# Performance work log

Hardware: AMD Instinct MI355X
Metric: run time of the kernel (lower is better)

Reference implementation:

```python
import jax, jax.numpy as jnp
import numpy as np

SR = 48000          # sample_rate
N = 24000           # num_samples (0.5 s)
NOISE_CUTOFF = 0.1  # torch.tensor([0.1]) in TransientGenerator


def exponential_envelope(n, attack, decay):
    # attack ramp times exponential decay over normalized time in [0, 1]
    t = jnp.linspace(0.0, 1.0, n)
    return (1.0 - jnp.exp(-attack * t)) * jnp.exp(-decay * t)


def one_pole_filter(x, cutoff):
    # y[n] = cutoff * x[n] + (1 - cutoff) * y[n-1]  (one-pole lowpass)
    def step(y, xi):
        y = cutoff * xi + (1.0 - cutoff) * y
        return y, y
    _, ys = jax.lax.scan(step, jnp.zeros((), x.dtype), x)
    return ys


def _drum_synth(parameters, noise_t, noise_n):
    t = jnp.linspace(0.0, 1.0, N)

    # ---- TransientGenerator (parameters[:5]) ----
    # params: attack (unused in original forward), decay, frequency, saturation, gain
    decay_t = parameters[1]
    freq_t = parameters[2]
    sat = parameters[3]
    gain_t = parameters[4]
    sine = jnp.sin(2.0 * jnp.pi * freq_t * t) * jnp.exp(-decay_t * t) * gain_t
    sine = jnp.tanh(sine * sat)
    filtered = one_pole_filter(noise_t, NOISE_CUTOFF)
    noise_comp = filtered * jnp.exp(-(decay_t * 20.0) * t) * (gain_t / 2.0)
    transient = sine + noise_comp  # [N]

    # ---- Resonator (parameters[5:8]): fractional-delay feedback recurrence ----
    freq_r = parameters[5]
    feedback = parameters[6]
    gain_r = parameters[7]
    delay_samples = SR / freq_r
    delayed = jnp.arange(N, dtype=jnp.float32) - delay_samples
    valid = (delayed >= 0).astype(jnp.float32)
    fl = jnp.clip(jnp.floor(delayed).astype(jnp.int32), 0, N - 1)
    ce = jnp.clip(fl + 1, 0, N - 1)
    frac = delayed - fl.astype(jnp.float32)  # computed after clamp, as in original

    out0 = jnp.zeros((N,), transient.dtype).at[0].set(transient[0])
    idx = jnp.arange(1, N, dtype=jnp.int32)

    def step(out, x):
        i, f_i, c_i, fr_i, vm_i, tr_i = x
        interp = (1.0 - fr_i) * out[f_i] + fr_i * out[c_i]
        out = out.at[i].set(tr_i + feedback * interp * vm_i)
        return out, None

    out, _ = jax.lax.scan(
        step, out0, (idx, fl[1:], ce[1:], frac[1:], valid[1:], transient[1:]))
    resonance = out * gain_r

    # ---- NoiseGenerator (parameters[8:]) ----
    attack_n = parameters[8]
    decay_n = parameters[9]
    gain_n = parameters[10]
    env = exponential_envelope(N, attack_n, decay_n)
    noise = noise_n * env * gain_n

    return transient + noise + resonance


def setup_inputs() -> dict:
    key = jax.random.key(0)
    k1, k2 = jax.random.split(key)
    # [attack_t, decay_t, freq_t, saturation, gain_t,
    #  freq_res, feedback, gain_res, attack_n, decay_n, gain_n]
    parameters = jnp.array(
        [0.01, 8.0, 60.0, 2.0, 1.0, 150.0, 0.95, 0.8, 50.0, 10.0, 0.3],
        dtype=jnp.float32)
    noise_t = jax.random.normal(k1, (N,), dtype=jnp.float32)
    noise_n = jax.random.normal(k2, (N,), dtype=jnp.float32)
    return {"parameters": parameters, "noise_t": noise_t, "noise_n": noise_n}


def reference(parameters, noise_t, noise_n):
    return _drum_synth(parameters, noise_t, noise_n)
```

## Files before the change

### kernel.cpp

```cpp
#include <hip/hip_runtime.h>
#include <math.h>


constexpr int   kN    = 24000;
constexpr float kInvT = 1.0f / 23999.0f;
constexpr int   kBT   = 64;

__global__ __launch_bounds__(kBT) void k1_transient(
    const float* __restrict__ params,
    const float* __restrict__ noise_t,
    float* __restrict__ tr)
{
  const int i = blockIdx.x * kBT + threadIdx.x;
  if (i >= kN) return;

  const float decay_t = params[1];
  const float freq_t  = params[2];
  const float sat     = params[3];
  const float gain_t  = params[4];

  float p0 = 0.f, p1 = 0.f, p2 = 0.f, p3 = 0.f;
  if (i >= 63) {
    #pragma unroll
    for (int j = 15; j >= 0; --j) {
      const int b = i - j;
      p0 = fmaf(0.9f, p0, noise_t[b     ]);
      p1 = fmaf(0.9f, p1, noise_t[b - 16]);
      p2 = fmaf(0.9f, p2, noise_t[b - 32]);
      p3 = fmaf(0.9f, p3, noise_t[b - 48]);
    }
  } else {
    #pragma unroll
    for (int j = 15; j >= 0; --j) {
      const int b = i - j;
      p0 = fmaf(0.9f, p0, (b      >= 0) ? noise_t[b     ] : 0.0f);
      p1 = fmaf(0.9f, p1, (b - 16 >= 0) ? noise_t[b - 16] : 0.0f);
      p2 = fmaf(0.9f, p2, (b - 32 >= 0) ? noise_t[b - 32] : 0.0f);
      p3 = fmaf(0.9f, p3, (b - 48 >= 0) ? noise_t[b - 48] : 0.0f);
    }
  }
  const float filtered = 0.1f * (p0 + 0.185302019f * p1
                                    + 0.034336838f * p2
                                    + 0.006362685f * p3);

  const float t = (float)i * kInvT;
  float s = __sinf(6.28318530718f * freq_t * t) * __expf(-decay_t * t) * gain_t;
  const float e2 = __expf(2.0f * sat * s);
  s = 1.0f - 2.0f / (e2 + 1.0f);
  const float nc = filtered * __expf(-decay_t * 20.0f * t) * (gain_t * 0.5f);
  tr[i] = s + nc;
}

__global__ __launch_bounds__(kBT) void k2_combine(
    const float* __restrict__ params,
    const float* __restrict__ noise_n,
    const float* __restrict__ tr,
    float* __restrict__ res_ws,
    float* __restrict__ out)
{
  const float fb  = params[6];
  const float gr  = params[7];
  const float att = params[8];
  const float dec = params[9];
  const float gn  = params[10];

  const float Dd = 48000.0f / params[5];
  const float fD = floorf(Dd);
  const int   B  = (int)fD;

  if (Dd == fD && B >= 1) {
    const int i = blockIdx.x * kBT + threadIdx.x;
    if (i >= kN) return;

    const float fb3 = fb * fb * fb;
    float res;

    if (B >= 320) {
      float p0 = 0.f, p1 = 0.f, p2 = 0.f;
      #pragma unroll
      for (int j = 24; j >= 0; --j) {
        const int i0 = i - 3 * j * B;
        const int i1 = i0 - B;
        const int i2 = i1 - B;
        p0 = fmaf(fb3, p0, (i0 >= 0) ? tr[i0] : 0.0f);
        p1 = fmaf(fb3, p1, (i1 >= 0) ? tr[i1] : 0.0f);
        p2 = fmaf(fb3, p2, (i2 >= 0) ? tr[i2] : 0.0f);
      }
      res = p0 + fb * p1 + (fb * fb) * p2;
    } else {
      const int Mmax = (kN - 1) / B;
      const int J    = Mmax / 3 + 1;
      float p0 = 0.f, p1 = 0.f, p2 = 0.f;
      for (int j = J - 1; j >= 0; --j) {
        const int i0 = i - 3 * j * B;
        const int i1 = i0 - B;
        const int i2 = i1 - B;
        p0 = fmaf(fb3, p0, (i0 >= 0) ? tr[i0] : 0.0f);
        p1 = fmaf(fb3, p1, (i1 >= 0) ? tr[i1] : 0.0f);
        p2 = fmaf(fb3, p2, (i2 >= 0) ? tr[i2] : 0.0f);
      }
      res = p0 + fb * p1 + (fb * fb) * p2;
    }

    const float t   = (float)i * kInvT;
    const float env = (1.0f - __expf(-att * t)) * __expf(-dec * t);
    out[i] = tr[i] + noise_n[i] * env * gn + gr * res;
  } else {
    if (blockIdx.x != 0) return;
    const int tid = threadIdx.x;
    const int Bb = (B < 1) ? 1 : B;
    const int nBands = (kN + Bb - 1) / Bb;
    for (int k = 0; k < nBands; ++k) {
      const int start = k * Bb;
      const int end = (start + Bb < kN) ? (start + Bb) : kN;
      if (tid == 0) {
        const int i = start;
        const float delayed = (float)i - Dd;
        const float validf = (delayed >= 0.0f) ? 1.0f : 0.0f;
        int fl = (int)floorf(delayed);
        fl = fl < 0 ? 0 : (fl > kN - 1 ? kN - 1 : fl);
        const int ce = fl + 1 > kN - 1 ? kN - 1 : fl + 1;
        const float frac = delayed - (float)fl;
        const float vfl = (fl <= start - 1) ? res_ws[fl] : 0.0f;
        const float vce = (ce <= start - 1) ? res_ws[ce] : 0.0f;
        res_ws[i] = tr[i] + fb * ((1.0f - frac) * vfl + frac * vce) * validf;
      }
      __syncthreads();
      for (int i = start + 1 + tid; i < end; i += kBT) {
        const float delayed = (float)i - Dd;
        const float validf = (delayed >= 0.0f) ? 1.0f : 0.0f;
        int fl = (int)floorf(delayed);
        fl = fl < 0 ? 0 : (fl > kN - 1 ? kN - 1 : fl);
        const int ce = fl + 1 > kN - 1 ? kN - 1 : fl + 1;
        const float frac = delayed - (float)fl;
        const float vfl = (fl <= start) ? res_ws[fl] : 0.0f;
        const float vce = (ce <= start) ? res_ws[ce] : 0.0f;
        res_ws[i] = tr[i] + fb * ((1.0f - frac) * vfl + frac * vce) * validf;
      }
      __syncthreads();
    }
    for (int i = tid; i < kN; i += kBT) {
      const float t   = (float)i * kInvT;
      const float env = (1.0f - __expf(-att * t)) * __expf(-dec * t);
      out[i] = tr[i] + noise_n[i] * env * gn + gr * res_ws[i];
    }
  }
}

extern "C" void kernel_launch(void* const* d_in, const int* in_sizes, int n_in,
                              void* d_out, int out_size, void* d_ws, size_t ws_size,
                              hipStream_t stream) {
  const float* params  = (const float*)d_in[0];
  const float* noise_t = (const float*)d_in[1];
  const float* noise_n = (const float*)d_in[2];
  float* out = (float*)d_out;
  float* ws_tr  = (float*)d_ws;
  float* ws_res = (float*)d_ws + kN;

  const int nb = (kN + kBT - 1) / kBT;
  k1_transient<<<nb, kBT, 0, stream>>>(params, noise_t, ws_tr);
  k2_combine<<<nb, kBT, 0, stream>>>(params, noise_n, ws_tr, ws_res, out);
}
```

Before: 63.01 us.

## Fuse transient and resonator kernels by recomputing transient at delayed taps

Merges the two kernels into one. Each thread recomputes the sine and filtered-noise transient terms at every delayed tap of its comb sum instead of reading a precomputed transient buffer. The noise term is truncated past a cutoff index where its exponential envelope is negligible, so the costly FIR evaluation runs only over a limited range of taps. This removes a kernel launch and the intermediate global buffer round trip, at the cost of much more redundant transcendental and FIR work per output and a small approximation from the truncation.

```diff
diff --git a/kernel.cpp b/kernel.cpp
--- a/kernel.cpp
+++ b/kernel.cpp
@@ -6,112 +6,120 @@
 constexpr float kInvT = 1.0f / 23999.0f;
 constexpr int   kBT   = 64;
 
-__global__ __launch_bounds__(kBT) void k1_transient(
+__device__ __forceinline__ float fir_filtered(const float* __restrict__ x, int k) {
+  float p0 = 0.f, p1 = 0.f, p2 = 0.f, p3 = 0.f;
+  if (k >= 63) {
+    #pragma unroll
+    for (int j = 15; j >= 0; --j) {
+      const int b = k - j;
+      p0 = fmaf(0.9f, p0, x[b     ]);
+      p1 = fmaf(0.9f, p1, x[b - 16]);
+      p2 = fmaf(0.9f, p2, x[b - 32]);
+      p3 = fmaf(0.9f, p3, x[b - 48]);
+    }
+  } else {
+    #pragma unroll
+    for (int j = 15; j >= 0; --j) {
+      const int b = k - j;
+      p0 = fmaf(0.9f, p0, (b      >= 0) ? x[b     ] : 0.0f);
+      p1 = fmaf(0.9f, p1, (b - 16 >= 0) ? x[b - 16] : 0.0f);
+      p2 = fmaf(0.9f, p2, (b - 32 >= 0) ? x[b - 32] : 0.0f);
+      p3 = fmaf(0.9f, p3, (b - 48 >= 0) ? x[b - 48] : 0.0f);
+    }
+  }
+  return 0.1f * (p0 + 0.185302019f * p1 + 0.034336838f * p2 + 0.006362685f * p3);
+}
+
+__device__ __forceinline__ float sine_part(int k, float decay_t, float freq_t,
+                                           float sat, float gain_t) {
+  const float t = (float)k * kInvT;
+  float s = __sinf(6.28318530718f * freq_t * t) * __expf(-decay_t * t) * gain_t;
+  const float e2 = __expf(2.0f * sat * s);
+  return 1.0f - 2.0f / (e2 + 1.0f);
+}
+
+__device__ __forceinline__ float noise_part(const float* __restrict__ noise_t,
+                                            int k, float decay_t, float gain_t) {
+  return fir_filtered(noise_t, k)
+       * __expf(-decay_t * 20.0f * (float)k * kInvT) * (gain_t * 0.5f);
+}
+
+__global__ __launch_bounds__(kBT) void k_fused(
     const float* __restrict__ params,
     const float* __restrict__ noise_t,
-    float* __restrict__ tr)
+    const float* __restrict__ noise_n,
+    float* __restrict__ ws_tr,
+    float* __restrict__ res_ws,
+    float* __restrict__ out)
 {
-  const int i = blockIdx.x * kBT + threadIdx.x;
-  if (i >= kN) return;
-
   const float decay_t = params[1];
   const float freq_t  = params[2];
   const float sat     = params[3];
   const float gain_t  = params[4];
-
-  float p0 = 0.f, p1 = 0.f, p2 = 0.f, p3 = 0.f;
-  if (i >= 63) {
-    #pragma unroll
-    for (int j = 15; j >= 0; --j) {
-      const int b = i - j;
-      p0 = fmaf(0.9f, p0, noise_t[b     ]);
-      p1 = fmaf(0.9f, p1, noise_t[b - 16]);
-      p2 = fmaf(0.9f, p2, noise_t[b - 32]);
-      p3 = fmaf(0.9f, p3, noise_t[b - 48]);
-    }
-  } else {
-    #pragma unroll
-    for (int j = 15; j >= 0; --j) {
-      const int b = i - j;
-      p0 = fmaf(0.9f, p0, (b      >= 0) ? noise_t[b     ] : 0.0f);
-      p1 = fmaf(0.9f, p1, (b - 16 >= 0) ? noise_t[b - 16] : 0.0f);
-      p2 = fmaf(0.9f, p2, (b - 32 >= 0) ? noise_t[b - 32] : 0.0f);
-      p3 = fmaf(0.9f, p3, (b - 48 >= 0) ? noise_t[b - 48] : 0.0f);
-    }
-  }
-  const float filtered = 0.1f * (p0 + 0.185302019f * p1
-                                    + 0.034336838f * p2
-                                    + 0.006362685f * p3);
-
-  const float t = (float)i * kInvT;
-  float s = __sinf(6.28318530718f * freq_t * t) * __expf(-decay_t * t) * gain_t;
-  const float e2 = __expf(2.0f * sat * s);
-  s = 1.0f - 2.0f / (e2 + 1.0f);
-  const float nc = filtered * __expf(-decay_t * 20.0f * t) * (gain_t * 0.5f);
-  tr[i] = s + nc;
-}
-
-__global__ __launch_bounds__(kBT) void k2_combine(
-    const float* __restrict__ params,
-    const float* __restrict__ noise_n,
-    const float* __restrict__ tr,
-    float* __restrict__ res_ws,
-    float* __restrict__ out)
-{
-  const float fb  = params[6];
-  const float gr  = params[7];
-  const float att = params[8];
-  const float dec = params[9];
-  const float gn  = params[10];
+  const float fb      = params[6];
+  const float gr      = params[7];
+  const float att     = params[8];
+  const float dec     = params[9];
+  const float gn      = params[10];
 
   const float Dd = 48000.0f / params[5];
   const float fD = floorf(Dd);
   const int   B  = (int)fD;
 
+  int kcut = kN;
+  if (decay_t > 0.0f) {
+    const float kc = 16.118f / (20.0f * decay_t) * 23999.0f;
+    kcut = (kc >= (float)kN) ? kN : ((int)kc + 1);
+  }
+
   if (Dd == fD && B >= 1) {
     const int i = blockIdx.x * kBT + threadIdx.x;
     if (i >= kN) return;
 
-    const float fb3 = fb * fb * fb;
-    float res;
+    const int Mmax = i / B;
+    int mlo = 0;
+    if (i - kcut + 1 > 0) mlo = (i - kcut + B) / B;
 
-    if (B >= 320) {
-      float p0 = 0.f, p1 = 0.f, p2 = 0.f;
-      #pragma unroll
-      for (int j = 24; j >= 0; --j) {
-        const int i0 = i - 3 * j * B;
-        const int i1 = i0 - B;
-        const int i2 = i1 - B;
-        p0 = fmaf(fb3, p0, (i0 >= 0) ? tr[i0] : 0.0f);
-        p1 = fmaf(fb3, p1, (i1 >= 0) ? tr[i1] : 0.0f);
-        p2 = fmaf(fb3, p2, (i2 >= 0) ? tr[i2] : 0.0f);
-      }
-      res = p0 + fb * p1 + (fb * fb) * p2;
-    } else {
-      const int Mmax = (kN - 1) / B;
-      const int J    = Mmax / 3 + 1;
-      float p0 = 0.f, p1 = 0.f, p2 = 0.f;
-      for (int j = J - 1; j >= 0; --j) {
-        const int i0 = i - 3 * j * B;
-        const int i1 = i0 - B;
-        const int i2 = i1 - B;
-        p0 = fmaf(fb3, p0, (i0 >= 0) ? tr[i0] : 0.0f);
-        p1 = fmaf(fb3, p1, (i1 >= 0) ? tr[i1] : 0.0f);
-        p2 = fmaf(fb3, p2, (i2 >= 0) ? tr[i2] : 0.0f);
-      }
-      res = p0 + fb * p1 + (fb * fb) * p2;
+    float s_sum = 0.0f, w = 1.0f, w_lo = 1.0f, s_direct = 0.0f;
+    #pragma unroll 4
+    for (int m = 0; m <= Mmax; ++m) {
+      const int k = i - m * B;
+      const float s = sine_part(k, decay_t, freq_t, sat, gain_t);
+      if (m == 0)   s_direct = s;
+      if (m == mlo) w_lo = w;
+      s_sum = fmaf(w, s, s_sum);
+      w *= fb;
     }
 
+    float f_sum = 0.0f, f_direct = 0.0f, wf = w_lo;
+    for (int m = mlo; m <= Mmax; ++m) {
+      const int k = i - m * B;
+      const float f = noise_part(noise_t, k, decay_t, gain_t);
+      if (m == 0) f_direct = f;
+      f_sum = fmaf(wf, f, f_sum);
+      wf *= fb;
+    }
+
+    const float tri = s_direct + f_direct;
+    const float res = s_sum + f_sum;
     const float t   = (float)i * kInvT;
     const float env = (1.0f - __expf(-att * t)) * __expf(-dec * t);
-    out[i] = tr[i] + noise_n[i] * env * gn + gr * res;
+    out[i] = tri + noise_n[i] * env * gn + gr * res;
   } else {
     if (blockIdx.x != 0) return;
     const int tid = threadIdx.x;
+
+    for (int k = tid; k < kN; k += kBT) {
+      float v = sine_part(k, decay_t, freq_t, sat, gain_t);
+      if (k < kcut) v += noise_part(noise_t, k, decay_t, gain_t);
+      ws_tr[k] = v;
+    }
+    __syncthreads();
+
     const int Bb = (B < 1) ? 1 : B;
     const int nBands = (kN + Bb - 1) / Bb;
-    for (int k = 0; k < nBands; ++k) {
-      const int start = k * Bb;
+    for (int kb = 0; kb < nBands; ++kb) {
+      const int start = kb * Bb;
       const int end = (start + Bb < kN) ? (start + Bb) : kN;
       if (tid == 0) {
         const int i = start;
@@ -123,7 +131,7 @@
         const float frac = delayed - (float)fl;
         const float vfl = (fl <= start - 1) ? res_ws[fl] : 0.0f;
         const float vce = (ce <= start - 1) ? res_ws[ce] : 0.0f;
-        res_ws[i] = tr[i] + fb * ((1.0f - frac) * vfl + frac * vce) * validf;
+        res_ws[i] = ws_tr[i] + fb * ((1.0f - frac) * vfl + frac * vce) * validf;
       }
       __syncthreads();
       for (int i = start + 1 + tid; i < end; i += kBT) {
@@ -135,14 +143,14 @@
         const float frac = delayed - (float)fl;
         const float vfl = (fl <= start) ? res_ws[fl] : 0.0f;
         const float vce = (ce <= start) ? res_ws[ce] : 0.0f;
-        res_ws[i] = tr[i] + fb * ((1.0f - frac) * vfl + frac * vce) * validf;
+        res_ws[i] = ws_tr[i] + fb * ((1.0f - frac) * vfl + frac * vce) * validf;
       }
       __syncthreads();
     }
     for (int i = tid; i < kN; i += kBT) {
       const float t   = (float)i * kInvT;
       const float env = (1.0f - __expf(-att * t)) * __expf(-dec * t);
-      out[i] = tr[i] + noise_n[i] * env * gn + gr * res_ws[i];
+      out[i] = ws_tr[i] + noise_n[i] * env * gn + gr * res_ws[i];
     }
   }
 }
@@ -158,6 +166,5 @@
   float* ws_res = (float*)d_ws + kN;
 
   const int nb = (kN + kBT - 1) / kBT;
-  k1_transient<<<nb, kBT, 0, stream>>>(params, noise_t, ws_tr);
-  k2_combine<<<nb, kBT, 0, stream>>>(params, noise_n, ws_tr, ws_res, out);
+  k_fused<<<nb, kBT, 0, stream>>>(params, noise_t, noise_n, ws_tr, ws_res, out);
 }
```

Measured after the change: 67.52 us. 7.2% more time.
